# Kernel tuning notes

Measured on AMD Instinct MI355X. Metric: run time of the kernel, lower is better.

The kernel has to match this reference:

```python
import jax, jax.numpy as jnp
import numpy as np
from jax import lax

B, P, GRID, NP = 16, 220, 4, 16
DIM, DEPTH, HEADS, DH, MLP, NC = 512, 6, 8, 64, 2048, 1000
EPS = 1e-5
SCALE = DH ** -0.5
FLAT = 64 * 16 * 16  # per-patch CNN output [64,16,16] flattened (c,p1,p2 order)


def setup_inputs() -> dict:
    key = jax.random.key(0)
    ks = iter(jax.random.split(key, 40))
    def n(shape, std):
        return jax.random.normal(next(ks), shape, dtype=jnp.float32) * std
    return {
        "img": jax.random.normal(next(ks), (B, 1, GRID * P, GRID * P), dtype=jnp.float32),
        "conv1_w": n((32, 1, 7, 7), (2.0 / 49) ** 0.5),
        "conv2_w": n((64, 32, 7, 7), (2.0 / (32 * 49)) ** 0.5),
        "conv3_w": n((64, 64, 7, 7), (2.0 / (64 * 49)) ** 0.5),
        "flat_w": n((FLAT, DIM), FLAT ** -0.5),
        "flat_b": jnp.zeros((DIM,), jnp.float32),
        "cls_token": n((1, 1, DIM), 0.02),
        "pos_emb": n((1, NP + 1, DIM), 0.02),
        "ln1_g": jnp.ones((DEPTH, DIM), jnp.float32),
        "ln1_b": jnp.zeros((DEPTH, DIM), jnp.float32),
        "qkv_w": n((DEPTH, DIM, 3 * HEADS * DH), DIM ** -0.5),
        "out_w": n((DEPTH, HEADS * DH, DIM), (HEADS * DH) ** -0.5),
        "out_b": jnp.zeros((DEPTH, DIM), jnp.float32),
        "ln2_g": jnp.ones((DEPTH, DIM), jnp.float32),
        "ln2_b": jnp.zeros((DEPTH, DIM), jnp.float32),
        "ff1_w": n((DEPTH, DIM, MLP), DIM ** -0.5),
        "ff1_b": jnp.zeros((DEPTH, MLP), jnp.float32),
        "ff2_w": n((DEPTH, MLP, DIM), MLP ** -0.5),
        "ff2_b": jnp.zeros((DEPTH, DIM), jnp.float32),
        "head_ln_g": jnp.ones((DIM,), jnp.float32),
        "head_ln_b": jnp.zeros((DIM,), jnp.float32),
        "head_w": n((DIM, NC), DIM ** -0.5),
        "head_b": jnp.zeros((NC,), jnp.float32),
    }


def _ln(x, g, b):
    m = jnp.mean(x, axis=-1, keepdims=True)
    v = jnp.mean(jnp.square(x - m), axis=-1, keepdims=True)
    return (x - m) * lax.rsqrt(v + EPS) * g + b


def _cnn(x, w1, w2, w3):
    def block(h, w):
        h = lax.conv_general_dilated(h, w, (2, 2), 'VALID',
                                     dimension_numbers=('NCHW', 'OIHW', 'NCHW'))
        h = jax.nn.relu(h)
        # MaxPool2d(kernel=7, stride=1, padding=1)
        return lax.reduce_window(h, -jnp.inf, lax.max, (1, 1, 7, 7), (1, 1, 1, 1),
                                 ((0, 0), (0, 0), (1, 1), (1, 1)))
    return block(block(block(x, w1), w2), w3)


def _forward(img, conv1_w, conv2_w, conv3_w, flat_w, flat_b, cls_token, pos_emb,
             ln1_g, ln1_b, qkv_w, out_w, out_b, ln2_g, ln2_b,
             ff1_w, ff1_b, ff2_w, ff2_b, head_ln_g, head_ln_b, head_w, head_b):
    # b c (h p1) (w p2) -> (b h w) 1 p1 p2 ; all patches batched through the CNN at once
    patches = img.reshape(B, 1, GRID, P, GRID, P).transpose(0, 2, 4, 3, 1, 5)
    patches = patches.reshape(B * NP, 1, P, P)
    feat = _cnn(patches, conv1_w, conv2_w, conv3_w).reshape(B, NP, FLAT)  # [B,NP,64*16*16]
    x = feat @ flat_w + flat_b                                            # [B,NP,DIM]
    x = jnp.concatenate([jnp.broadcast_to(cls_token, (B, 1, DIM)), x], axis=1) + pos_emb
    N = NP + 1

    def layer(x, p):
        g1, b1, qw, ow, ob, g2, b2, w1, fb1, w2, fb2 = p
        h = _ln(x, g1, b1)
        q, k, v = jnp.split(h @ qw, 3, axis=-1)
        def heads(t):
            return t.reshape(B, N, HEADS, DH).transpose(0, 2, 1, 3)  # b h n d
        q, k, v = heads(q), heads(k), heads(v)
        attn = jax.nn.softmax(jnp.einsum('bhqd,bhkd->bhqk', q, k) * SCALE, axis=-1)
        o = jnp.einsum('bhqk,bhkd->bhqd', attn, v).transpose(0, 2, 1, 3).reshape(B, N, HEADS * DH)
        x = x + o @ ow + ob
        h2 = _ln(x, g2, b2)
        x = x + jax.nn.gelu(h2 @ w1 + fb1, approximate=False) @ w2 + fb2
        return x, None

    x, _ = lax.scan(layer, x, (ln1_g, ln1_b, qkv_w, out_w, out_b,
                               ln2_g, ln2_b, ff1_w, ff1_b, ff2_w, ff2_b))
    cls = _ln(x[:, 0], head_ln_g, head_ln_b)
    return cls @ head_w + head_b  # [B, NC]


def reference(img, conv1_w, conv2_w, conv3_w, flat_w, flat_b, cls_token, pos_emb,
              ln1_g, ln1_b, qkv_w, out_w, out_b, ln2_g, ln2_b,
              ff1_w, ff1_b, ff2_w, ff2_b, head_ln_g, head_ln_b, head_w, head_b):
    return _forward(img, conv1_w, conv2_w, conv3_w, flat_w, flat_b, cls_token, pos_emb,
                    ln1_g, ln1_b, qkv_w, out_w, out_b, ln2_g, ln2_b,
                    ff1_w, ff1_b, ff2_w, ff2_b, head_ln_g, head_ln_b, head_w, head_b)
```

## Files before the change

kernel.cpp:

```cpp
#include <hip/hip_runtime.h>
#include <hip/hip_bf16.h>


typedef __hip_bfloat16 bf16;
typedef __attribute__((ext_vector_type(8))) short short8;
typedef __attribute__((ext_vector_type(4))) float floatx4;

#define CHUNK 64

union U8 { int4 v; unsigned short s[8]; };
__device__ inline void umax8(U8& a, const U8& b){
  #pragma unroll
  for (int j = 0; j < 8; j++) a.s[j] = (a.s[j] > b.s[j]) ? a.s[j] : b.s[j];
}
union U4 { uint2 v; unsigned short s[4]; };
__device__ inline void umax4(U4& a, const U4& b){
  #pragma unroll
  for (int j = 0; j < 4; j++) a.s[j] = (a.s[j] > b.s[j]) ? a.s[j] : b.s[j];
}

__global__ __launch_bounds__(256) void prep_w2(const float* __restrict__ w,
                                               bf16* __restrict__ w2b)
{
  int idx = blockIdx.x*256 + threadIdx.x;
  if (idx >= 49*64*32) return;
  int ic = idx & 31; int t = idx >> 5; int oc = t & 63; int kk = t >> 6;
  int ky = kk/7, kx = kk - ky*7;
  w2b[idx] = __float2bfloat16(w[((oc*32+ic)*7+ky)*7+kx]);
}

__global__ __launch_bounds__(256) void prep_w3(const float* __restrict__ w,
                                               bf16* __restrict__ w3b)
{
  int idx = blockIdx.x*256 + threadIdx.x;
  if (idx >= 49*2*64*32) return;
  int ic_l = idx & 31; int t = idx >> 5; int oc = t & 63; int t2 = t >> 6;
  int kx = t2 % 7; int t3 = t2 / 7; int kc = t3 & 1; int ky = t3 >> 1;
  w3b[idx] = __float2bfloat16(w[((oc*64 + kc*32 + ic_l)*7+ky)*7+kx]);
}

__global__ __launch_bounds__(256) void prep_pack(
    const float* __restrict__ src, bf16* __restrict__ dst,
    int K8, int N, int total)
{
  int idx = blockIdx.x*256 + threadIdx.x;
  if (idx >= total) return;
  int n = idx % N; int t = idx / N; int k8 = t % K8; int l = t / K8;
  const float* s = src + ((size_t)l*K8*8 + (size_t)k8*8)*N + n;
  union { bf16 h[8]; int4 v; } pk;
  #pragma unroll
  for (int j = 0; j < 8; j++) pk.h[j] = __float2bfloat16(s[(size_t)j*N]);
  *(int4*)(dst + (((size_t)l*K8 + k8)*N + n)*8) = pk.v;
}

__global__ __launch_bounds__(256) void prep_pack_flat(
    const float* __restrict__ src, bf16* __restrict__ hi, bf16* __restrict__ lo)
{
  int idx = blockIdx.x*256 + threadIdx.x;
  if (idx >= 2048*512) return;
  int n = idx & 511; int k8 = idx >> 9;
  const float* s = src + (size_t)k8*8*512 + n;
  union { bf16 h[8]; int4 v; } ph, pl;
  #pragma unroll
  for (int j = 0; j < 8; j++){
    float w = s[(size_t)j*512];
    bf16 h = __float2bfloat16(w);
    ph.h[j] = h;
    pl.h[j] = __float2bfloat16(w - __bfloat162float(h));
  }
  size_t o = (size_t)idx*8;
  *(int4*)(hi + o) = ph.v;
  *(int4*)(lo + o) = pl.v;
}

__global__ __launch_bounds__(256) void k1a_conv1(
    const float* __restrict__ img, const float* __restrict__ w,
    bf16* __restrict__ cbuf, int n_base)
{
  __shared__ __align__(16) float in_s[15*224];
  __shared__ float w_s[32*58];
  const int band = blockIdx.x;
  const int n = blockIdx.y;
  const int ng = n_base + n;
  const int r0 = band*5;
  const int ir0 = 2*r0;
  const int b = ng>>4, gh = (ng>>2)&3, gw = ng&3;
  const float* ibase = img + b*774400 + (gh*220)*880 + gw*220;

  for (int idx = threadIdx.x; idx < 15*56; idx += 256){
    int r = idx/56, cq = idx - r*56; int c = cq*4;
    int gr = ir0 + r;
    float4 v = (c < 220 && gr < 220) ? *(const float4*)(ibase + gr*880 + c)
                                     : make_float4(0.f,0.f,0.f,0.f);
    *(float4*)&in_s[r*224 + c] = v;
  }
  for (int idx = threadIdx.x; idx < 32*56; idx += 256){
    int oc = idx/56, k = idx - oc*56; int ky = k>>3, kx = k&7;
    w_s[oc*58 + k] = (kx < 7) ? w[oc*49 + ky*7 + kx] : 0.f;
  }
  __syncthreads();

  const int grp = threadIdx.x & 7;
  const int sp  = threadIdx.x >> 3;
  const int cgc = (sp < 26) ? sp : 26;
  const int nrows = (107 - r0 < 5) ? (107 - r0) : 5;

  float acc[5][4][4] = {};
  #pragma unroll 1
  for (int ky = 0; ky < 7; ky++){
    float wk[4][7];
    #pragma unroll
    for (int oc = 0; oc < 4; oc++)
      #pragma unroll
      for (int kx = 0; kx < 7; kx++)
        wk[oc][kx] = w_s[(grp*4+oc)*58 + ky*8 + kx];
    #pragma unroll
    for (int i = 0; i < 5; i++){
      if (i < nrows){
        const float* ip = &in_s[(2*i+ky)*224 + 8*cgc];
        float iv[13];
        *(float4*)&iv[0] = *(const float4*)ip;
        *(float4*)&iv[4] = *(const float4*)(ip+4);
        *(float4*)&iv[8] = *(const float4*)(ip+8);
        iv[12] = ip[12];
        #pragma unroll
        for (int oc = 0; oc < 4; oc++)
          #pragma unroll
          for (int kx = 0; kx < 7; kx++)
            #pragma unroll
            for (int j = 0; j < 4; j++)
              acc[i][oc][j] += iv[2*j+kx]*wk[oc][kx];
      }
    }
  }

  #pragma unroll
  for (int i = 0; i < 5; i++){
    if (i < nrows){
      int y = r0 + i;
      #pragma unroll
      for (int j = 0; j < 4; j++){
        int col = 4*sp + j;
        if (col < 107){
          union { unsigned short s[4]; uint2 u; } pk;
          #pragma unroll
          for (int oc = 0; oc < 4; oc++){
            bf16 hv = __float2bfloat16(fmaxf(acc[i][oc][j], 0.f));
            pk.s[oc] = *(unsigned short*)&hv;
          }
          *(uint2*)(cbuf + (((size_t)(n*8+grp)*107 + y)*107 + col)*4) = pk.u;
        }
      }
    }
  }
}

__global__ __launch_bounds__(256) void k1b_pool1(
    const bf16* __restrict__ cbuf, bf16* __restrict__ pool1, int n_pool_base)
{
  __shared__ uint2 in4[19*107];
  __shared__ uint2 ht4[19*103];
  const int s = blockIdx.x, g = blockIdx.y, n = blockIdx.z;
  const int p0 = s*13;
  const int PR = (103 - p0 < 13) ? (103 - p0) : 13;
  const int NR = PR + 6;
  const uint2* src = (const uint2*)cbuf + (size_t)(n*8+g)*107*107;

  for (int t = threadIdx.x; t < NR*107; t += 256){
    int r = t/107, c = t - r*107;
    int gr = p0 - 1 + r;
    gr = (gr < 0) ? 0 : ((gr > 106) ? 106 : gr);
    in4[t] = src[gr*107 + c];
  }
  __syncthreads();
  for (int t = threadIdx.x; t < NR*103; t += 256){
    int r = t/103, c = t - r*103;
    U4 m; m.v = in4[r*107 + ((c > 0) ? c-1 : 0)];
    #pragma unroll
    for (int d = 0; d < 6; d++){
      U4 v; v.v = in4[r*107 + ((c+d < 106) ? c+d : 106)];
      umax4(m, v);
    }
    ht4[r*103 + c] = m.v;
  }
  __syncthreads();
  uint2* dst = (uint2*)pool1;
  const size_t plane = ((size_t)(n_pool_base + n)*4 + (g>>1))*10609;
  const int h = g & 1;
  for (int t = threadIdx.x; t < PR*103; t += 256){
    int pr = t/103, c = t - pr*103;
    U4 m; m.v = ht4[pr*103 + c];
    #pragma unroll
    for (int d = 1; d < 7; d++){
      U4 v; v.v = ht4[(pr+d)*103 + c];
      umax4(m, v);
    }
    dst[(plane + (size_t)(p0+pr)*103 + c)*2 + h] = m.v;
  }
}

__global__ __launch_bounds__(256) void k2_conv2(
    const bf16* __restrict__ pool1,
    const bf16* __restrict__ w2b,
    bf16* __restrict__ conv2out)
{
  __shared__ __align__(16) bf16 in_s[7*2*52*36];
  const int n = blockIdx.y, pb = blockIdx.x;
  const int wv = threadIdx.x >> 6, lane = threadIdx.x & 63;
  const int li = lane & 15, lg = lane >> 4;
  const int p0 = pb*256;
  const int y0 = p0/49;

  int pyv[4], pxv[4], poff[4]; bool pmask[4];
  #pragma unroll
  for (int t = 0; t < 4; t++){
    int p = p0 + wv*64 + t*16 + li;
    pmask[t] = (p <= 2400);
    int pc = min(p, 2400);
    int yy = pc/49, xx = pc - yy*49;
    pyv[t] = yy; pxv[t] = xx;
    poff[t] = ((yy - y0)*2*52 + xx)*36;
  }
  floatx4 acc[4][4];
  #pragma unroll
  for (int a = 0; a < 4; a++)
    #pragma unroll
    for (int t = 0; t < 4; t++) acc[a][t] = (floatx4){0.f,0.f,0.f,0.f};

  const unsigned short* pbase = (const unsigned short*)pool1;
  for (int ky = 0; ky < 7; ky++){
    __syncthreads();
    for (int idx = threadIdx.x; idx < 7*103*4; idx += 256){
      int q = idx & 3; int t2 = idx >> 2; int c = t2 % 103; int r = t2/103;
      int gr = min(2*(y0+r)+ky, 102);
      *(int4*)&in_s[((r*2 + (c&1))*52 + (c>>1))*36 + q*8] =
        *(const int4*)(pbase + (((size_t)n*4 + q)*10609 + (size_t)gr*103 + c)*8);
    }
    __syncthreads();
    #pragma unroll
    for (int kx = 0; kx < 7; kx++){
      short8 a[4];
      const bf16* wp = w2b + (ky*7+kx)*64*32;
      #pragma unroll
      for (int ot = 0; ot < 4; ot++)
        a[ot] = *(const short8*)(wp + (ot*16 + li)*32 + lg*8);
      int koff = ((kx&1)*52 + (kx>>1))*36 + lg*8;
      #pragma unroll
      for (int t = 0; t < 4; t++){
        short8 bfr = *(const short8*)(&in_s[poff[t] + koff]);
        #pragma unroll
        for (int ot = 0; ot < 4; ot++)
          acc[ot][t] = __builtin_amdgcn_mfma_f32_16x16x32_bf16(a[ot], bfr, acc[ot][t], 0, 0, 0);
      }
    }
  }
  #pragma unroll
  for (int t = 0; t < 4; t++){
    if (!pmask[t]) continue;
    bf16* dst = conv2out + (((long)n*49 + pyv[t])*49 + pxv[t])*64 + lg*4;
    #pragma unroll
    for (int ot = 0; ot < 4; ot++){
      union { bf16 h[4]; uint2 u; } pk;
      #pragma unroll
      for (int v = 0; v < 4; v++)
        pk.h[v] = __float2bfloat16(fmaxf(acc[ot][t][v], 0.f));
      *(uint2*)(dst + ot*16) = pk.u;
    }
  }
}

__global__ __launch_bounds__(256) void k3a_hmax(
    const bf16* __restrict__ cin, bf16* __restrict__ tmp)
{
  int idx = blockIdx.x*256 + threadIdx.x;
  int cg = idx & 7; int t = idx >> 3; int x = t % 45; int t2 = t / 45;
  int y = t2 % 49; int n = t2 / 49;
  const int4* row = (const int4*)(cin + ((long)(n*49 + y)*49)*64) + cg;
  U8 m; m.v = make_int4(0,0,0,0);
  int lo = max(x-1, 0), hi = min(x+5, 48);
  for (int cx = lo; cx <= hi; cx++){ U8 v; v.v = row[cx*8]; umax8(m, v); }
  *((int4*)(tmp + ((long)(n*49 + y)*45 + x)*64) + cg) = m.v;
}

__global__ __launch_bounds__(256) void k3b_vmax(
    const bf16* __restrict__ tmp, bf16* __restrict__ pout, int n_base)
{
  int idx = blockIdx.x*256 + threadIdx.x;
  int cg = idx & 7; int t = idx >> 3; int x = t % 45; int t2 = t / 45;
  int y = t2 % 45; int n = t2 / 45;
  U8 m; m.v = make_int4(0,0,0,0);
  int lo = max(y-1, 0), hi = min(y+5, 48);
  for (int cy = lo; cy <= hi; cy++){
    U8 v; v.v = *((const int4*)(tmp + ((long)(n*49 + cy)*45 + x)*64) + cg);
    umax8(m, v);
  }
  *((int4*)(pout + (long)(n_base+n)*129600 + (y*45 + x)*64) + cg) = m.v;
}

__global__ __launch_bounds__(256) void k4_conv3(
    const bf16* __restrict__ pool2,
    const bf16* __restrict__ w3b,
    bf16* __restrict__ conv3out)
{
  __shared__ __align__(16) bf16 in_s[10*2*24*40];
  const int n = blockIdx.y, pb = blockIdx.x;
  const int wv = threadIdx.x >> 6, lane = threadIdx.x & 63;
  const int li = lane & 15, lg = lane >> 4;
  const int y0 = pb*10;

  int pyv[4], pxv[4], poff[4]; bool pmask[4];
  #pragma unroll
  for (int t = 0; t < 4; t++){
    int pl = wv*64 + t*16 + li;
    pmask[t] = (pl < 200);
    int p = pb*200 + min(pl, 199);
    int yy = p/20, xx = p - yy*20;
    pyv[t] = yy; pxv[t] = xx;
    poff[t] = ((yy - y0)*2*24 + xx)*40;
  }
  floatx4 acc[4][4];
  #pragma unroll
  for (int a = 0; a < 4; a++)
    #pragma unroll
    for (int t = 0; t < 4; t++) acc[a][t] = (floatx4){0.f,0.f,0.f,0.f};

  for (int ky = 0; ky < 7; ky++){
    for (int kc = 0; kc < 2; kc++){
      __syncthreads();
      for (int idx = threadIdx.x; idx < 10*45*4; idx += 256){
        int q = idx & 3; int t2 = idx >> 2; int c = t2 % 45; int r = t2/45;
        int gr = 2*(y0+r)+ky;
        const bf16* src = pool2 + (((long)n*45 + gr)*45 + c)*64 + kc*32 + q*8;
        bf16* dst = &in_s[((r*2 + (c&1))*24 + (c>>1))*40 + q*8];
        *(int4*)dst = *(const int4*)src;
      }
      __syncthreads();
      #pragma unroll
      for (int kx = 0; kx < 7; kx++){
        short8 a[4];
        const bf16* wp = w3b + ((ky*2+kc)*7 + kx)*64*32;
        #pragma unroll
        for (int ot = 0; ot < 4; ot++)
          a[ot] = *(const short8*)(wp + (ot*16 + li)*32 + lg*8);
        int koff = ((kx&1)*24 + (kx>>1))*40 + lg*8;
        #pragma unroll
        for (int t = 0; t < 4; t++){
          short8 bfr = *(const short8*)(&in_s[poff[t] + koff]);
          #pragma unroll
          for (int ot = 0; ot < 4; ot++)
            acc[ot][t] = __builtin_amdgcn_mfma_f32_16x16x32_bf16(a[ot], bfr, acc[ot][t], 0, 0, 0);
        }
      }
    }
  }
  #pragma unroll
  for (int t = 0; t < 4; t++){
    if (!pmask[t]) continue;
    bf16* dst = conv3out + (((long)n*20 + pyv[t])*20 + pxv[t])*64 + lg*4;
    #pragma unroll
    for (int ot = 0; ot < 4; ot++){
      union { bf16 h[4]; uint2 u; } pk;
      #pragma unroll
      for (int v = 0; v < 4; v++)
        pk.h[v] = __float2bfloat16(fmaxf(acc[ot][t][v], 0.f));
      *(uint2*)(dst + ot*16) = pk.u;
    }
  }
}

__global__ __launch_bounds__(256) void k5_pool3(
    const bf16* __restrict__ cin, bf16* __restrict__ feat)
{
  __shared__ int4 in_p[3200];
  __shared__ int4 ht[2560];
  const int n = blockIdx.x;
  const int4* src = (const int4*)(cin + (long)n*25600);
  for (int i = threadIdx.x; i < 3200; i += 256) in_p[i] = src[i];
  __syncthreads();
  for (int i = threadIdx.x; i < 2560; i += 256){
    int cg = i & 7; int t = i >> 3; int x = t & 15; int y = t >> 4;
    U8 m; m.v = make_int4(0,0,0,0);
    int lo = max(x-1, 0), hi = min(x+5, 19);
    for (int cx = lo; cx <= hi; cx++){ U8 v; v.v = in_p[(y*20+cx)*8 + cg]; umax8(m, v); }
    ht[(y*16+x)*8 + cg] = m.v;
  }
  __syncthreads();
  unsigned short* dst = (unsigned short*)(feat + (long)n*16384);
  for (int i = threadIdx.x; i < 2048; i += 256){
    int px = i & 15; int py = (i >> 4) & 15; int cg = i >> 8;
    U8 m; m.v = make_int4(0,0,0,0);
    int lo = max(py-1, 0), hi = min(py+5, 19);
    for (int cy = lo; cy <= hi; cy++){ U8 v; v.v = ht[(cy*16+px)*8 + cg]; umax8(m, v); }
    #pragma unroll
    for (int j = 0; j < 8; j++)
      dst[(cg*8+j)*256 + py*16 + px] = m.s[j];
  }
}

__global__ __launch_bounds__(256) void k6_init_x(
    const float* __restrict__ cls, const float* __restrict__ pos,
    const float* __restrict__ flat_b, float* __restrict__ x)
{
  int idx = blockIdx.x*256 + threadIdx.x;
  int d = idx & 511; int row = idx >> 9;
  int tt = row % 17;
  x[idx] = (tt == 0) ? (cls[d] + pos[d]) : (flat_b[d] + pos[tt*512 + d]);
}

__global__ __launch_bounds__(256) void k6_flat_mfma(
    const bf16* __restrict__ feat, const bf16* __restrict__ Whi,
    const bf16* __restrict__ Wlo, float* __restrict__ x)
{
  const int wv = threadIdx.x >> 6, lane = threadIdx.x & 63;
  const int li = lane & 15, lg = lane >> 4;
  const int m0 = blockIdx.x*64 + wv*16;
  const int nb = blockIdx.y*64;
  const int kb = blockIdx.z*2048;
  floatx4 acc[4];
  #pragma unroll
  for (int t = 0; t < 4; t++) acc[t] = (floatx4){0.f,0.f,0.f,0.f};

  const bf16* arow = feat + (size_t)(m0+li)*16384 + kb + lg*8;
  for (int k0 = 0; k0 < 2048; k0 += 32){
    short8 a = *(const short8*)(arow + k0);
    size_t wo = ((size_t)((kb + k0) >> 3) + lg)*512 + nb + li;
    const bf16* wh = Whi + wo*8;
    const bf16* wl = Wlo + wo*8;
    #pragma unroll
    for (int t = 0; t < 4; t++){
      short8 bh = *(const short8*)(wh + t*128);
      acc[t] = __builtin_amdgcn_mfma_f32_16x16x32_bf16(a, bh, acc[t], 0, 0, 0);
    }
    #pragma unroll
    for (int t = 0; t < 4; t++){
      short8 bl = *(const short8*)(wl + t*128);
      acc[t] = __builtin_amdgcn_mfma_f32_16x16x32_bf16(a, bl, acc[t], 0, 0, 0);
    }
  }
  #pragma unroll
  for (int t = 0; t < 4; t++){
    int col = nb + t*16 + li;
    #pragma unroll
    for (int v = 0; v < 4; v++){
      int m = m0 + lg*4 + v;
      int row = (m>>4)*17 + 1 + (m&15);
      atomicAdd(&x[row*512 + col], acc[t][v]);
    }
  }
}

__global__ __launch_bounds__(256) void ln_kernel(
    const float* __restrict__ in, const float* __restrict__ g,
    const float* __restrict__ b, float* __restrict__ out,
    int in_stride, int out_stride)
{
  int row = blockIdx.x;
  const float* p = in + (long)row*in_stride;
  float v0 = p[threadIdx.x], v1 = p[threadIdx.x+256];
  __shared__ float red[4]; __shared__ float stat;
  float s = v0+v1;
  #pragma unroll
  for (int o = 32; o >= 1; o >>= 1) s += __shfl_down(s, o);
  int lane = threadIdx.x & 63, wv = threadIdx.x >> 6;
  if (lane == 0) red[wv] = s;
  __syncthreads();
  if (threadIdx.x == 0) stat = (red[0]+red[1]+red[2]+red[3])*(1.0f/512.0f);
  __syncthreads();
  float m = stat;
  float d0 = v0-m, d1 = v1-m;
  float q = d0*d0 + d1*d1;
  #pragma unroll
  for (int o = 32; o >= 1; o >>= 1) q += __shfl_down(q, o);
  __syncthreads();
  if (lane == 0) red[wv] = q;
  __syncthreads();
  if (threadIdx.x == 0) stat = rsqrtf((red[0]+red[1]+red[2]+red[3])*(1.0f/512.0f) + 1e-5f);
  __syncthreads();
  float rstd = stat;
  out[(long)row*out_stride + threadIdx.x]     = d0*rstd*g[threadIdx.x]     + b[threadIdx.x];
  out[(long)row*out_stride + threadIdx.x+256] = d1*rstd*g[threadIdx.x+256] + b[threadIdx.x+256];
}

__global__ __launch_bounds__(256) void ln_bf16(
    const float* __restrict__ in, const float* __restrict__ g,
    const float* __restrict__ b, bf16* __restrict__ out)
{
  int row = blockIdx.x;
  const float* p = in + (long)row*512;
  float v0 = p[threadIdx.x], v1 = p[threadIdx.x+256];
  __shared__ float red[4]; __shared__ float stat;
  float s = v0+v1;
  #pragma unroll
  for (int o = 32; o >= 1; o >>= 1) s += __shfl_down(s, o);
  int lane = threadIdx.x & 63, wv = threadIdx.x >> 6;
  if (lane == 0) red[wv] = s;
  __syncthreads();
  if (threadIdx.x == 0) stat = (red[0]+red[1]+red[2]+red[3])*(1.0f/512.0f);
  __syncthreads();
  float m = stat;
  float d0 = v0-m, d1 = v1-m;
  float q = d0*d0 + d1*d1;
  #pragma unroll
  for (int o = 32; o >= 1; o >>= 1) q += __shfl_down(q, o);
  __syncthreads();
  if (lane == 0) red[wv] = q;
  __syncthreads();
  if (threadIdx.x == 0) stat = rsqrtf((red[0]+red[1]+red[2]+red[3])*(1.0f/512.0f) + 1e-5f);
  __syncthreads();
  float rstd = stat;
  out[(long)row*512 + threadIdx.x]     = __float2bfloat16(d0*rstd*g[threadIdx.x]     + b[threadIdx.x]);
  out[(long)row*512 + threadIdx.x+256] = __float2bfloat16(d1*rstd*g[threadIdx.x+256] + b[threadIdx.x+256]);
}

template<int NT>
__global__ __launch_bounds__(256) void tail_gemm(
    const bf16* __restrict__ A, const bf16* __restrict__ Wp,
    const float* __restrict__ bias, const float* res,
    float* outf, bf16* outb, int N, int K, int dogelu)
{
  const int wv = threadIdx.x >> 6, lane = threadIdx.x & 63;
  const int li = lane & 15, lg = lane >> 4;
  const int m0 = blockIdx.x * 16;
  const int nb = blockIdx.y * (64*NT) + wv * (16*NT);
  floatx4 acc[NT];
  #pragma unroll
  for (int t = 0; t < NT; t++) acc[t] = (floatx4){0.f,0.f,0.f,0.f};
  const bf16* arow = A + (size_t)(m0+li)*K + lg*8;
  for (int k0 = 0; k0 < K; k0 += 32){
    short8 a = *(const short8*)(arow + k0);
    const bf16* wrow = Wp + ((size_t)((k0>>3) + lg) * N + nb + li) * 8;
    #pragma unroll
    for (int t = 0; t < NT; t++){
      short8 bfr = *(const short8*)(wrow + t*128);
      acc[t] = __builtin_amdgcn_mfma_f32_16x16x32_bf16(a, bfr, acc[t], 0, 0, 0);
    }
  }
  #pragma unroll
  for (int t = 0; t < NT; t++){
    int col = nb + t*16 + li;
    #pragma unroll
    for (int v = 0; v < 4; v++){
      int row = m0 + lg*4 + v;
      float val = acc[t][v];
      if (bias) val += bias[col];
      if (dogelu) val = 0.5f*val*(1.0f + erff(val*0.70710678118654752f));
      if (res) val += res[(size_t)row*N + col];
      if (outf) outf[(size_t)row*N + col] = val;
      else      outb[(size_t)row*N + col] = __float2bfloat16(val);
    }
  }
}

__global__ __launch_bounds__(256) void gemm_rows(
    const float* __restrict__ A, const float* __restrict__ W,
    const float* __restrict__ bias, const float* __restrict__ res,
    float* __restrict__ out, int M, int N, int K, int dogelu)
{
  __shared__ float A_s[16][33];
  __shared__ __align__(16) float W_s[32][68];
  const int m0 = blockIdx.x*16, n0 = blockIdx.y*64;
  const int r = threadIdx.x>>4, c0 = (threadIdx.x&15)*4;
  float acc[4] = {};
  for (int k0 = 0; k0 < K; k0 += 32){
    __syncthreads();
    for (int i = 0; i < 2; i++){ int id = threadIdx.x + i*256; int rr = id>>5, kk = id&31;
      A_s[rr][kk] = (m0+rr < M) ? A[(long)(m0+rr)*K + k0+kk] : 0.f; }
    for (int i = 0; i < 8; i++){ int id = threadIdx.x + i*256; int kk = id>>6, c = id&63;
      W_s[kk][c] = (n0+c < N) ? W[(long)(k0+kk)*N + n0+c] : 0.f; }
    __syncthreads();
    #pragma unroll
    for (int kk = 0; kk < 32; kk++){
      float a = A_s[r][kk];
      float4 w4 = *(const float4*)&W_s[kk][c0];
      acc[0]+=a*w4.x; acc[1]+=a*w4.y; acc[2]+=a*w4.z; acc[3]+=a*w4.w;
    }
  }
  if (m0+r < M){
    int row = m0+r;
    for (int j = 0; j < 4; j++){
      int c = n0+c0+j;
      if (c < N){
        float v = acc[j];
        if (bias) v += bias[c];
        if (dogelu) v = 0.5f*v*(1.0f + erff(v*0.70710678118654752f));
        if (res) v += res[(long)row*N + c];
        out[(long)row*N + c] = v;
      }
    }
  }
}

__global__ __launch_bounds__(128) void attn_kernel(
    const float* __restrict__ qkv, bf16* __restrict__ obuf)
{
  const int b = blockIdx.x >> 3, h = blockIdx.x & 7;
  __shared__ float q_s[17][65], k_s[17][65], v_s[17][65], s_s[17][18];
  for (int idx = threadIdx.x; idx < 17*64; idx += 128){
    int i = idx>>6, d = idx&63;
    const float* base = qkv + (long)(b*17+i)*1536 + h*64 + d;
    q_s[i][d] = base[0]; k_s[i][d] = base[512]; v_s[i][d] = base[1024];
  }
  __syncthreads();
  for (int idx = threadIdx.x; idx < 289; idx += 128){
    int i = idx/17, j = idx - i*17;
    float s = 0.f;
    for (int d = 0; d < 64; d++) s += q_s[i][d]*k_s[j][d];
    s_s[i][j] = s*0.125f;
  }
  __syncthreads();
  if (threadIdx.x < 17){
    int i = threadIdx.x;
    float m = -1e30f;
    for (int j = 0; j < 17; j++) m = fmaxf(m, s_s[i][j]);
    float sum = 0.f;
    for (int j = 0; j < 17; j++){ float e = expf(s_s[i][j]-m); s_s[i][j] = e; sum += e; }
    float inv = 1.0f/sum;
    for (int j = 0; j < 17; j++) s_s[i][j] *= inv;
  }
  __syncthreads();
  for (int idx = threadIdx.x; idx < 17*64; idx += 128){
    int i = idx>>6, d = idx&63;
    float o = 0.f;
    for (int j = 0; j < 17; j++) o += s_s[i][j]*v_s[j][d];
    obuf[(long)(b*17+i)*512 + h*64 + d] = __float2bfloat16(o);
  }
}

extern "C" void kernel_launch(void* const* d_in, const int* in_sizes, int n_in,
                              void* d_out, int out_size, void* d_ws, size_t ws_size,
                              hipStream_t stream) {
  const float* img      = (const float*)d_in[0];
  const float* conv1_w  = (const float*)d_in[1];
  const float* conv2_w  = (const float*)d_in[2];
  const float* conv3_w  = (const float*)d_in[3];
  const float* flat_w   = (const float*)d_in[4];
  const float* flat_b   = (const float*)d_in[5];
  const float* cls_tok  = (const float*)d_in[6];
  const float* pos_emb  = (const float*)d_in[7];
  const float* ln1_g    = (const float*)d_in[8];
  const float* ln1_b    = (const float*)d_in[9];
  const float* qkv_w    = (const float*)d_in[10];
  const float* out_w    = (const float*)d_in[11];
  const float* out_b    = (const float*)d_in[12];
  const float* ln2_g    = (const float*)d_in[13];
  const float* ln2_b    = (const float*)d_in[14];
  const float* ff1_w    = (const float*)d_in[15];
  const float* ff1_b    = (const float*)d_in[16];
  const float* ff2_w    = (const float*)d_in[17];
  const float* ff2_b    = (const float*)d_in[18];
  const float* hln_g    = (const float*)d_in[19];
  const float* hln_b    = (const float*)d_in[20];
  const float* head_w   = (const float*)d_in[21];
  const float* head_b   = (const float*)d_in[22];

  char* ws = (char*)d_ws;
  size_t off = 0;
  auto alloc = [&](size_t bytes) -> void* {
    void* p = ws + off; off += (bytes + 255) & ~(size_t)255; return p;
  };
  bf16* pool1    = (bf16*)alloc((size_t)CHUNK*8*103*103*4*2);
  bf16* conv2out = (bf16*)alloc((size_t)CHUNK*49*49*64*2);
  bf16* pool2    = (bf16*)alloc((size_t)256*45*45*64*2);
  bf16* feat     = (bf16*)alloc((size_t)256*16384*2);
  bf16* w2b      = (bf16*)alloc((size_t)49*64*32*2);
  bf16* w3b      = (bf16*)alloc((size_t)49*2*64*32*2);
  float* x       = (float*)alloc((size_t)139264*4);
  bf16*  hb      = (bf16*)alloc((size_t)139264*2);
  float* qkvb    = (float*)alloc((size_t)417792*4);
  bf16*  obufb   = (bf16*)alloc((size_t)139264*2);
  bf16*  ffbufb  = (bf16*)alloc((size_t)557056*2);
  float* hcls    = (float*)alloc((size_t)8192*4);
  bf16* tmp3     = pool1;
  bf16* conv3out = pool1;
  bf16* qkvp  = pool1;
  bf16* outwp = qkvp  + (size_t)6*512*1536;
  bf16* ff1p  = outwp + (size_t)6*512*512;
  bf16* ff2p  = ff1p  + (size_t)6*512*2048;
  bf16* fwhi  = conv2out;
  bf16* fwlo  = pool2;

  const size_t cb_per_n = (size_t)8*107*107*4*2;
  int SUB; bf16* cbuf;
  if (ws_size >= off + 64*cb_per_n)      { SUB = 64; cbuf = (bf16*)alloc(64*cb_per_n); }
  else if (ws_size >= off + 32*cb_per_n) { SUB = 32; cbuf = (bf16*)alloc(32*cb_per_n); }
  else { SUB = 16; cbuf = conv2out; }
  (void)in_sizes; (void)n_in; (void)out_size;

  prep_w2<<<392, 256, 0, stream>>>(conv2_w, w2b);
  prep_w3<<<784, 256, 0, stream>>>(conv3_w, w3b);

  for (int cb = 0; cb < 256; cb += CHUNK){
    for (int sb = 0; sb < CHUNK; sb += SUB){
      k1a_conv1<<<dim3(22, SUB), 256, 0, stream>>>(img, conv1_w, cbuf, cb + sb);
      k1b_pool1<<<dim3(8, 8, SUB), 256, 0, stream>>>(cbuf, pool1, sb);
    }
    k2_conv2     <<<dim3(10,CHUNK), 256, 0, stream>>>(pool1, w2b, conv2out);
    k3a_hmax     <<<(CHUNK*49*45*8)/256, 256, 0, stream>>>(conv2out, tmp3);
    k3b_vmax     <<<(CHUNK*45*45*8)/256, 256, 0, stream>>>(tmp3, pool2, cb);
  }
  k4_conv3<<<dim3(2,256), 256, 0, stream>>>(pool2, w3b, conv3out);
  k5_pool3<<<256, 256, 0, stream>>>(conv3out, feat);

  prep_pack_flat<<<4096, 256, 0, stream>>>(flat_w, fwhi, fwlo);
  prep_pack<<<(6*64*1536+255)/256, 256, 0, stream>>>(qkv_w, qkvp, 64, 1536, 6*64*1536);
  prep_pack<<<(6*64*512 +255)/256, 256, 0, stream>>>(out_w, outwp, 64, 512,  6*64*512);
  prep_pack<<<(6*64*2048+255)/256, 256, 0, stream>>>(ff1_w, ff1p, 64, 2048, 6*64*2048);
  prep_pack<<<(6*256*512+255)/256, 256, 0, stream>>>(ff2_w, ff2p, 256, 512, 6*256*512);

  k6_init_x    <<<544,         256, 0, stream>>>(cls_tok, pos_emb, flat_b, x);
  k6_flat_mfma <<<dim3(4,8,8), 256, 0, stream>>>(feat, fwhi, fwlo, x);

  for (int l = 0; l < 6; l++){
    ln_bf16<<<272, 256, 0, stream>>>(x, ln1_g + l*512, ln1_b + l*512, hb);
    tail_gemm<4><<<dim3(17,6), 256, 0, stream>>>(hb, qkvp + (size_t)l*786432,
                                                 nullptr, nullptr, qkvb, nullptr, 1536, 512, 0);
    attn_kernel<<<128, 128, 0, stream>>>(qkvb, obufb);
    tail_gemm<1><<<dim3(17,8), 256, 0, stream>>>(obufb, outwp + (size_t)l*262144,
                                                 out_b + l*512, x, x, nullptr, 512, 512, 0);
    ln_bf16<<<272, 256, 0, stream>>>(x, ln2_g + l*512, ln2_b + l*512, hb);
    tail_gemm<4><<<dim3(17,8), 256, 0, stream>>>(hb, ff1p + (size_t)l*1048576,
                                                 ff1_b + l*2048, nullptr, nullptr, ffbufb, 2048, 512, 1);
    tail_gemm<1><<<dim3(17,8), 256, 0, stream>>>(ffbufb, ff2p + (size_t)l*1048576,
                                                 ff2_b + l*512, x, x, nullptr, 512, 2048, 0);
  }

  ln_kernel<<<16, 256, 0, stream>>>(x, hln_g, hln_b, hcls, 17*512, 512);
  gemm_rows<<<dim3(1,16), 256, 0, stream>>>(hcls, head_w, head_b, nullptr,
                                            (float*)d_out, 16, 1000, 512, 0);
}
```

Measured before the change: 1.701 ms.

## Reuse staged input rows across ky in conv2 via ring buffer ordering

Conv2 now walks the kernel rows in parity order (even ky, then odd ky) and keeps the staged input rows in a 7-slot ring buffer in shared memory. After the first full stage for each parity, only one new row is loaded per step instead of seven. This is meant to cut redundant global-to-LDS traffic in the conv2 kernel. The cost is per-step modulo slot arithmetic for the LDS offsets and a loop that is no longer unrolled.

Result: faster. 1.599 ms (-6.0%).

```diff
diff --git a/kernel.cpp b/kernel.cpp
--- a/kernel.cpp
+++ b/kernel.cpp
@@ -211,7 +211,7 @@
   const int p0 = pb*256;
   const int y0 = p0/49;
 
-  int pyv[4], pxv[4], poff[4]; bool pmask[4];
+  int pyv[4], pxv[4]; bool pmask[4];
   #pragma unroll
   for (int t = 0; t < 4; t++){
     int p = p0 + wv*64 + t*16 + li;
@@ -219,7 +219,6 @@
     int pc = min(p, 2400);
     int yy = pc/49, xx = pc - yy*49;
     pyv[t] = yy; pxv[t] = xx;
-    poff[t] = ((yy - y0)*2*52 + xx)*36;
   }
   floatx4 acc[4][4];
   #pragma unroll
@@ -228,15 +227,34 @@
     for (int t = 0; t < 4; t++) acc[a][t] = (floatx4){0.f,0.f,0.f,0.f};
 
   const unsigned short* pbase = (const unsigned short*)pool1;
-  for (int ky = 0; ky < 7; ky++){
+
+  auto stage_rows = [&](int e0, int cnt, int par){
+    for (int idx = threadIdx.x; idx < cnt*103*4; idx += 256){
+      int q = idx & 3; int t2 = idx >> 2; int ri = t2/103; int c = t2 - ri*103;
+      int e = e0 + ri;
+      int slot = e % 7;
+      int gr = min(2*e + par, 102);
+      *(int4*)&in_s[((slot*2 + (c&1))*52 + (c>>1))*36 + q*8] =
+        *(const int4*)(pbase + (((size_t)n*4 + q)*10609 + (size_t)gr*103 + c)*8);
+    }
+  };
+
+  const int kyseq[7] = {0,2,4,6,1,3,5};
+  #pragma unroll 1
+  for (int ks = 0; ks < 7; ks++){
+    int ky = kyseq[ks];
+    int kyh = ky >> 1, par = ky & 1;
     __syncthreads();
-    for (int idx = threadIdx.x; idx < 7*103*4; idx += 256){
-      int q = idx & 3; int t2 = idx >> 2; int c = t2 % 103; int r = t2/103;
-      int gr = min(2*(y0+r)+ky, 102);
-      *(int4*)&in_s[((r*2 + (c&1))*52 + (c>>1))*36 + q*8] =
-        *(const int4*)(pbase + (((size_t)n*4 + q)*10609 + (size_t)gr*103 + c)*8);
-    }
+    if (ks == 0 || ks == 4) stage_rows(y0, 7, par);
+    else                    stage_rows(y0 + 6 + kyh, 1, par);
     __syncthreads();
+    int poff[4];
+    #pragma unroll
+    for (int t = 0; t < 4; t++){
+      int e = pyv[t] + kyh;
+      int slot = e % 7;
+      poff[t] = (slot*2*52 + pxv[t])*36;
+    }
     #pragma unroll
     for (int kx = 0; kx < 7; kx++){
       short8 a[4];
```
